# Kernel optimization log

Measured on AMD Instinct MI355X. Metric: run time of the kernel, lower is better.

Reference implementation:

```python
import jax, jax.numpy as jnp
import numpy as np

B, H, S, D = 1, 16, 4096, 64

def setup_inputs() -> dict:
    key = jax.random.key(0)
    kq, kk, kv = jax.random.split(key, 3)
    q = jax.random.normal(kq, (B, H, S, D), dtype=jnp.float32)
    k = jax.random.normal(kk, (B, H, S, D), dtype=jnp.float32)
    v = jax.random.normal(kv, (B, H, S, D), dtype=jnp.float32)
    return {"q": q, "k": k, "v": v}

def reference(q, k, v):
    # attn = q @ k^T  -> [B,H,S,S]; output = attn @ v -> [B,H,S,D]
    attn = jnp.einsum('bhqd,bhkd->bhqk', q, k)
    out = jnp.einsum('bhqk,bhkd->bhqd', attn, v)
    return out
```

## Files before the change

### kernel.cpp

```cpp
#include <hip/hip_runtime.h>
#include <stddef.h>


#define SLEN 4096
#define DIM  64
#define NH   16
#define CH   32
#define RPC  (SLEN / CH)

typedef float f4v __attribute__((ext_vector_type(4)));

__global__ __launch_bounds__(256) void kvT_partial(const float* __restrict__ K,
                                                   const float* __restrict__ V,
                                                   float* __restrict__ P) {
    const int c = blockIdx.x;
    const int h = blockIdx.y;
    const int t = threadIdx.x;
    const int i = t >> 4;
    const int j = t & 15;

    __shared__ float Ks[32][64];
    __shared__ float Vs[32][64];

    const f4v* K4 = (const f4v*)(K + ((size_t)h * SLEN + (size_t)c * RPC) * DIM);
    const f4v* V4 = (const f4v*)(V + ((size_t)h * SLEN + (size_t)c * RPC) * DIM);

    float acc[4][4] = {{0.f,0.f,0.f,0.f},{0.f,0.f,0.f,0.f},
                       {0.f,0.f,0.f,0.f},{0.f,0.f,0.f,0.f}};

    f4v kst[2], vst[2];
    #pragma unroll
    for (int u = 0; u < 2; ++u) {
        int idx = u * 256 + t, row = idx >> 4, c4 = idx & 15;
        kst[u] = K4[row * 16 + c4];
        vst[u] = V4[row * 16 + c4];
    }

    for (int tile = 0; tile < 4; ++tile) {
        __syncthreads();
        #pragma unroll
        for (int u = 0; u < 2; ++u) {
            int idx = u * 256 + t, row = idx >> 4, c4 = idx & 15;
            *(f4v*)&Ks[row][c4 * 4] = kst[u];
            *(f4v*)&Vs[row][c4 * 4] = vst[u];
        }
        __syncthreads();

        if (tile < 3) {
            #pragma unroll
            for (int u = 0; u < 2; ++u) {
                int idx = u * 256 + t, row = idx >> 4, c4 = idx & 15;
                kst[u] = K4[((tile + 1) * 32 + row) * 16 + c4];
                vst[u] = V4[((tile + 1) * 32 + row) * 16 + c4];
            }
        }

        #pragma unroll
        for (int s = 0; s < 32; ++s) {
            f4v kf = *(const f4v*)&Ks[s][i * 4];
            f4v vf = *(const f4v*)&Vs[s][j * 4];
            #pragma unroll
            for (int a = 0; a < 4; ++a)
                #pragma unroll
                for (int b = 0; b < 4; ++b)
                    acc[a][b] = fmaf(kf[a], vf[b], acc[a][b]);
        }
    }

    float* Pc = P + ((size_t)h * CH + c) * (DIM * DIM);
    #pragma unroll
    for (int a = 0; a < 4; ++a) {
        f4v r;
        r[0] = acc[a][0]; r[1] = acc[a][1]; r[2] = acc[a][2]; r[3] = acc[a][3];
        *(f4v*)&Pc[(i * 4 + a) * DIM + j * 4] = r;
    }
}

__global__ __launch_bounds__(256) void reduceM(const float* __restrict__ P,
                                               float* __restrict__ M) {
    const int q = blockIdx.x;
    const int h = blockIdx.y;
    const int t = threadIdx.x;
    const int off = q * 256 + t;

    const f4v* Ph = (const f4v*)(P + (size_t)h * CH * DIM * DIM);
    f4v sum; sum[0] = 0.f; sum[1] = 0.f; sum[2] = 0.f; sum[3] = 0.f;
    #pragma unroll
    for (int c = 0; c < CH; ++c) {
        f4v x = Ph[(size_t)c * (DIM * DIM / 4) + off];
        sum[0] += x[0]; sum[1] += x[1]; sum[2] += x[2]; sum[3] += x[3];
    }
    ((f4v*)(M + (size_t)h * DIM * DIM))[off] = sum;
}

__global__ __launch_bounds__(256) void qm_kernel(const float* __restrict__ Q,
                                                 const float* __restrict__ M,
                                                 float* __restrict__ O) {
    const int chunk = blockIdx.x;
    const int h     = blockIdx.y;
    const int t     = threadIdx.x;
    const int i     = t >> 4;
    const int j     = t & 15;

    __shared__ float Qs[64][68];
    __shared__ float Ms[64][64];

    const f4v* Q4 = (const f4v*)(Q + ((size_t)h * SLEN + (size_t)chunk * 64) * DIM);
    const f4v* M4 = (const f4v*)(M + (size_t)h * DIM * DIM);

    #pragma unroll
    for (int it = 0; it < 4; ++it) {
        int idx = it * 256 + t;
        int row = idx >> 4;
        int c4  = idx & 15;
        *(f4v*)&Qs[row][c4 * 4] = Q4[idx];
        *(f4v*)&Ms[row][c4 * 4] = M4[idx];
    }
    __syncthreads();

    float acc[4][4] = {{0.f,0.f,0.f,0.f},{0.f,0.f,0.f,0.f},
                       {0.f,0.f,0.f,0.f},{0.f,0.f,0.f,0.f}};

    for (int d0 = 0; d0 < DIM; d0 += 4) {
        f4v qf[4], mf[4];
        #pragma unroll
        for (int a = 0; a < 4; ++a)
            qf[a] = *(const f4v*)&Qs[i * 4 + a][d0];
        #pragma unroll
        for (int cc = 0; cc < 4; ++cc)
            mf[cc] = *(const f4v*)&Ms[d0 + cc][j * 4];
        #pragma unroll
        for (int a = 0; a < 4; ++a)
            #pragma unroll
            for (int cc = 0; cc < 4; ++cc)
                #pragma unroll
                for (int b = 0; b < 4; ++b)
                    acc[a][b] = fmaf(qf[a][cc], mf[cc][b], acc[a][b]);
    }

    f4v* O4 = (f4v*)O;
    #pragma unroll
    for (int a = 0; a < 4; ++a) {
        f4v res;
        res[0] = acc[a][0]; res[1] = acc[a][1]; res[2] = acc[a][2]; res[3] = acc[a][3];
        O4[((size_t)h * SLEN + (size_t)chunk * 64 + i * 4 + a) * (DIM / 4) + j] = res;
    }
}

extern "C" void kernel_launch(void* const* d_in, const int* in_sizes, int n_in,
                              void* d_out, int out_size, void* d_ws, size_t ws_size,
                              hipStream_t stream) {
    const float* q = (const float*)d_in[0];
    const float* k = (const float*)d_in[1];
    const float* v = (const float*)d_in[2];
    float* out = (float*)d_out;
    float* P = (float*)d_ws;
    float* M = P + (size_t)NH * CH * DIM * DIM;

    kvT_partial<<<dim3(CH, NH), 256, 0, stream>>>(k, v, P);
    reduceM<<<dim3(4, NH), 256, 0, stream>>>(P, M);
    qm_kernel<<<dim3(64, NH), 256, 0, stream>>>(q, M, out);
}
```

Measured before the change: 109.2 us.

## Fuse KV partial, reduction and QM into one kernel with atomic counters

Replaces the three launches (K^T V partial products, chunk reduction, Q·M) with one persistent-style kernel of 512 blocks. Blocks sync per head through global atomic counters and spin-waits: every block publishes its partial, four blocks per head reduce into M, then every block computes two Q chunks. The aim is to remove launch gaps between stages and to overlap the Q prefetch with the wait. It relies on all 512 blocks being co-resident to avoid deadlock, and adds a memset plus spin-polling overhead.

```diff
diff --git a/kernel.cpp b/kernel.cpp
--- a/kernel.cpp
+++ b/kernel.cpp
@@ -10,140 +10,174 @@
 
 typedef float f4v __attribute__((ext_vector_type(4)));
 
-__global__ __launch_bounds__(256) void kvT_partial(const float* __restrict__ K,
-                                                   const float* __restrict__ V,
-                                                   float* __restrict__ P) {
-    const int c = blockIdx.x;
-    const int h = blockIdx.y;
+__device__ __forceinline__ int atomic_read(int* p) { return atomicAdd(p, 0); }
+
+__global__ __launch_bounds__(256, 2) void fused_attn(
+    const float* __restrict__ Q, const float* __restrict__ K,
+    const float* __restrict__ V, float* __restrict__ O,
+    float* __restrict__ P, float* __restrict__ Mbuf, int* __restrict__ cnt)
+{
+    const int b = blockIdx.x;
     const int t = threadIdx.x;
     const int i = t >> 4;
     const int j = t & 15;
+    const int h = b >> 5;
+    const int c = b & 31;
 
-    __shared__ float Ks[32][64];
-    __shared__ float Vs[32][64];
+    __shared__ float smem[64 * 68 + 64 * 64];
 
-    const f4v* K4 = (const f4v*)(K + ((size_t)h * SLEN + (size_t)c * RPC) * DIM);
-    const f4v* V4 = (const f4v*)(V + ((size_t)h * SLEN + (size_t)c * RPC) * DIM);
+    {
+        float (*Ks)[64] = reinterpret_cast<float(*)[64]>(smem);
+        float (*Vs)[64] = reinterpret_cast<float(*)[64]>(smem + 32 * 64);
 
-    float acc[4][4] = {{0.f,0.f,0.f,0.f},{0.f,0.f,0.f,0.f},
-                       {0.f,0.f,0.f,0.f},{0.f,0.f,0.f,0.f}};
+        const f4v* K4 = (const f4v*)(K + ((size_t)h * SLEN + (size_t)c * RPC) * DIM);
+        const f4v* V4 = (const f4v*)(V + ((size_t)h * SLEN + (size_t)c * RPC) * DIM);
 
-    f4v kst[2], vst[2];
-    #pragma unroll
-    for (int u = 0; u < 2; ++u) {
-        int idx = u * 256 + t, row = idx >> 4, c4 = idx & 15;
-        kst[u] = K4[row * 16 + c4];
-        vst[u] = V4[row * 16 + c4];
-    }
+        float acc[4][4] = {{0.f,0.f,0.f,0.f},{0.f,0.f,0.f,0.f},
+                           {0.f,0.f,0.f,0.f},{0.f,0.f,0.f,0.f}};
 
-    for (int tile = 0; tile < 4; ++tile) {
-        __syncthreads();
+        f4v kst[2], vst[2];
         #pragma unroll
         for (int u = 0; u < 2; ++u) {
             int idx = u * 256 + t, row = idx >> 4, c4 = idx & 15;
-            *(f4v*)&Ks[row][c4 * 4] = kst[u];
-            *(f4v*)&Vs[row][c4 * 4] = vst[u];
+            kst[u] = K4[row * 16 + c4];
+            vst[u] = V4[row * 16 + c4];
+        }
+
+        for (int tile = 0; tile < 4; ++tile) {
+            __syncthreads();
+            #pragma unroll
+            for (int u = 0; u < 2; ++u) {
+                int idx = u * 256 + t, row = idx >> 4, c4 = idx & 15;
+                *(f4v*)&Ks[row][c4 * 4] = kst[u];
+                *(f4v*)&Vs[row][c4 * 4] = vst[u];
+            }
+            __syncthreads();
+
+            if (tile < 3) {
+                #pragma unroll
+                for (int u = 0; u < 2; ++u) {
+                    int idx = u * 256 + t, row = idx >> 4, c4 = idx & 15;
+                    kst[u] = K4[((tile + 1) * 32 + row) * 16 + c4];
+                    vst[u] = V4[((tile + 1) * 32 + row) * 16 + c4];
+                }
+            }
+
+            #pragma unroll
+            for (int s = 0; s < 32; ++s) {
+                f4v kf = *(const f4v*)&Ks[s][i * 4];
+                f4v vf = *(const f4v*)&Vs[s][j * 4];
+                #pragma unroll
+                for (int a = 0; a < 4; ++a)
+                    #pragma unroll
+                    for (int bb = 0; bb < 4; ++bb)
+                        acc[a][bb] = fmaf(kf[a], vf[bb], acc[a][bb]);
+            }
+        }
+
+        float* Pc = P + ((size_t)h * CH + c) * (DIM * DIM);
+        #pragma unroll
+        for (int a = 0; a < 4; ++a) {
+            f4v r;
+            r[0] = acc[a][0]; r[1] = acc[a][1]; r[2] = acc[a][2]; r[3] = acc[a][3];
+            *(f4v*)&Pc[(i * 4 + a) * DIM + j * 4] = r;
+        }
+    }
+    __threadfence();
+    __syncthreads();
+    if (t == 0) atomicAdd(&cnt[h], 1);
+
+    if (c < 4) {
+        if (t == 0) {
+            while (atomic_read(&cnt[h]) < CH) __builtin_amdgcn_s_sleep(2);
+        }
+        __syncthreads();
+        __threadfence();
+
+        const f4v* Ph = (const f4v*)(P + (size_t)h * CH * DIM * DIM);
+        const int off = c * 256 + t;
+        f4v sum; sum[0] = 0.f; sum[1] = 0.f; sum[2] = 0.f; sum[3] = 0.f;
+        #pragma unroll
+        for (int cc = 0; cc < CH; ++cc) {
+            f4v x = Ph[cc * (DIM * DIM / 4) + off];
+            sum[0] += x[0]; sum[1] += x[1]; sum[2] += x[2]; sum[3] += x[3];
+        }
+        ((f4v*)(Mbuf + (size_t)h * DIM * DIM))[off] = sum;
+
+        __threadfence();
+        __syncthreads();
+        if (t == 0) atomicAdd(&cnt[NH + h], 1);
+    }
+
+    {
+        const f4v* Q4_0 = (const f4v*)(Q + ((size_t)h * SLEN + (size_t)(c * 2) * 64) * DIM);
+        f4v qst[4];
+        #pragma unroll
+        for (int it = 0; it < 4; ++it) qst[it] = Q4_0[it * 256 + t];
+
+        if (t == 0) {
+            while (atomic_read(&cnt[NH + h]) < 4) __builtin_amdgcn_s_sleep(2);
+        }
+        __syncthreads();
+        __threadfence();
+
+        float (*Qs)[68] = reinterpret_cast<float(*)[68]>(smem);
+        float (*Ms)[64] = reinterpret_cast<float(*)[64]>(smem + 64 * 68);
+        const f4v* M4 = (const f4v*)(Mbuf + (size_t)h * DIM * DIM);
+        f4v* O4 = (f4v*)O;
+
+        #pragma unroll
+        for (int it = 0; it < 4; ++it) {
+            int idx = it * 256 + t, row = idx >> 4, c4 = idx & 15;
+            *(f4v*)&Ms[row][c4 * 4] = M4[idx];
+            *(f4v*)&Qs[row][c4 * 4] = qst[it];
         }
         __syncthreads();
 
-        if (tile < 3) {
+        for (int sub = 0; sub < 2; ++sub) {
+            const int chunk = c * 2 + sub;
+
+            if (sub) {
+                const f4v* Q4 = (const f4v*)(Q + ((size_t)h * SLEN + (size_t)chunk * 64) * DIM);
+                f4v q2[4];
+                #pragma unroll
+                for (int it = 0; it < 4; ++it) q2[it] = Q4[it * 256 + t];
+                __syncthreads();
+                #pragma unroll
+                for (int it = 0; it < 4; ++it) {
+                    int idx = it * 256 + t, row = idx >> 4, c4 = idx & 15;
+                    *(f4v*)&Qs[row][c4 * 4] = q2[it];
+                }
+                __syncthreads();
+            }
+
+            float acc[4][4] = {{0.f,0.f,0.f,0.f},{0.f,0.f,0.f,0.f},
+                               {0.f,0.f,0.f,0.f},{0.f,0.f,0.f,0.f}};
+
+            for (int d0 = 0; d0 < DIM; d0 += 4) {
+                f4v qf[4], mf[4];
+                #pragma unroll
+                for (int a = 0; a < 4; ++a)
+                    qf[a] = *(const f4v*)&Qs[i * 4 + a][d0];
+                #pragma unroll
+                for (int cc = 0; cc < 4; ++cc)
+                    mf[cc] = *(const f4v*)&Ms[d0 + cc][j * 4];
+                #pragma unroll
+                for (int a = 0; a < 4; ++a)
+                    #pragma unroll
+                    for (int cc = 0; cc < 4; ++cc)
+                        #pragma unroll
+                        for (int bb = 0; bb < 4; ++bb)
+                            acc[a][bb] = fmaf(qf[a][cc], mf[cc][bb], acc[a][bb]);
+            }
+
             #pragma unroll
-            for (int u = 0; u < 2; ++u) {
-                int idx = u * 256 + t, row = idx >> 4, c4 = idx & 15;
-                kst[u] = K4[((tile + 1) * 32 + row) * 16 + c4];
-                vst[u] = V4[((tile + 1) * 32 + row) * 16 + c4];
+            for (int a = 0; a < 4; ++a) {
+                f4v res;
+                res[0] = acc[a][0]; res[1] = acc[a][1]; res[2] = acc[a][2]; res[3] = acc[a][3];
+                O4[((size_t)h * SLEN + (size_t)chunk * 64 + i * 4 + a) * (DIM / 4) + j] = res;
             }
         }
-
-        #pragma unroll
-        for (int s = 0; s < 32; ++s) {
-            f4v kf = *(const f4v*)&Ks[s][i * 4];
-            f4v vf = *(const f4v*)&Vs[s][j * 4];
-            #pragma unroll
-            for (int a = 0; a < 4; ++a)
-                #pragma unroll
-                for (int b = 0; b < 4; ++b)
-                    acc[a][b] = fmaf(kf[a], vf[b], acc[a][b]);
-        }
-    }
-
-    float* Pc = P + ((size_t)h * CH + c) * (DIM * DIM);
-    #pragma unroll
-    for (int a = 0; a < 4; ++a) {
-        f4v r;
-        r[0] = acc[a][0]; r[1] = acc[a][1]; r[2] = acc[a][2]; r[3] = acc[a][3];
-        *(f4v*)&Pc[(i * 4 + a) * DIM + j * 4] = r;
-    }
-}
-
-__global__ __launch_bounds__(256) void reduceM(const float* __restrict__ P,
-                                               float* __restrict__ M) {
-    const int q = blockIdx.x;
-    const int h = blockIdx.y;
-    const int t = threadIdx.x;
-    const int off = q * 256 + t;
-
-    const f4v* Ph = (const f4v*)(P + (size_t)h * CH * DIM * DIM);
-    f4v sum; sum[0] = 0.f; sum[1] = 0.f; sum[2] = 0.f; sum[3] = 0.f;
-    #pragma unroll
-    for (int c = 0; c < CH; ++c) {
-        f4v x = Ph[(size_t)c * (DIM * DIM / 4) + off];
-        sum[0] += x[0]; sum[1] += x[1]; sum[2] += x[2]; sum[3] += x[3];
-    }
-    ((f4v*)(M + (size_t)h * DIM * DIM))[off] = sum;
-}
-
-__global__ __launch_bounds__(256) void qm_kernel(const float* __restrict__ Q,
-                                                 const float* __restrict__ M,
-                                                 float* __restrict__ O) {
-    const int chunk = blockIdx.x;
-    const int h     = blockIdx.y;
-    const int t     = threadIdx.x;
-    const int i     = t >> 4;
-    const int j     = t & 15;
-
-    __shared__ float Qs[64][68];
-    __shared__ float Ms[64][64];
-
-    const f4v* Q4 = (const f4v*)(Q + ((size_t)h * SLEN + (size_t)chunk * 64) * DIM);
-    const f4v* M4 = (const f4v*)(M + (size_t)h * DIM * DIM);
-
-    #pragma unroll
-    for (int it = 0; it < 4; ++it) {
-        int idx = it * 256 + t;
-        int row = idx >> 4;
-        int c4  = idx & 15;
-        *(f4v*)&Qs[row][c4 * 4] = Q4[idx];
-        *(f4v*)&Ms[row][c4 * 4] = M4[idx];
-    }
-    __syncthreads();
-
-    float acc[4][4] = {{0.f,0.f,0.f,0.f},{0.f,0.f,0.f,0.f},
-                       {0.f,0.f,0.f,0.f},{0.f,0.f,0.f,0.f}};
-
-    for (int d0 = 0; d0 < DIM; d0 += 4) {
-        f4v qf[4], mf[4];
-        #pragma unroll
-        for (int a = 0; a < 4; ++a)
-            qf[a] = *(const f4v*)&Qs[i * 4 + a][d0];
-        #pragma unroll
-        for (int cc = 0; cc < 4; ++cc)
-            mf[cc] = *(const f4v*)&Ms[d0 + cc][j * 4];
-        #pragma unroll
-        for (int a = 0; a < 4; ++a)
-            #pragma unroll
-            for (int cc = 0; cc < 4; ++cc)
-                #pragma unroll
-                for (int b = 0; b < 4; ++b)
-                    acc[a][b] = fmaf(qf[a][cc], mf[cc][b], acc[a][b]);
-    }
-
-    f4v* O4 = (f4v*)O;
-    #pragma unroll
-    for (int a = 0; a < 4; ++a) {
-        f4v res;
-        res[0] = acc[a][0]; res[1] = acc[a][1]; res[2] = acc[a][2]; res[3] = acc[a][3];
-        O4[((size_t)h * SLEN + (size_t)chunk * 64 + i * 4 + a) * (DIM / 4) + j] = res;
     }
 }
 
@@ -154,10 +188,12 @@
     const float* k = (const float*)d_in[1];
     const float* v = (const float*)d_in[2];
     float* out = (float*)d_out;
-    float* P = (float*)d_ws;
-    float* M = P + (size_t)NH * CH * DIM * DIM;
 
-    kvT_partial<<<dim3(CH, NH), 256, 0, stream>>>(k, v, P);
-    reduceM<<<dim3(4, NH), 256, 0, stream>>>(P, M);
-    qm_kernel<<<dim3(64, NH), 256, 0, stream>>>(q, M, out);
+    int*   cnt = (int*)d_ws;
+    float* P   = (float*)d_ws + 64;
+    float* M   = P + (size_t)NH * CH * DIM * DIM;
+
+    hipMemsetAsync(d_ws, 0, 256, stream);
+
+    fused_attn<<<dim3(512), dim3(256), 0, stream>>>(q, k, v, out, P, M, cnt);
 }
```

New measurement: 278.6 us. +155.1%, slower.
